# Optimization experiments

Hardware: AMD Instinct MI355X
Metric: run time of the kernel (lower is better)

## Reference

```python
import jax, jax.numpy as jnp
import numpy as np

PROJ_DIM = 8192
INPUT_DIM = 512
THRESH = 1e-08


def _signed_sqrt(x):
    return jnp.sign(x) * jnp.sqrt(jnp.abs(x))


def _make_sketch_matrix(key, input_dim, proj_dim):
    kh, ks = jax.random.split(key)
    h = jax.random.randint(kh, (input_dim,), 0, proj_dim)
    s = jnp.sign(jax.random.uniform(ks, (input_dim,), minval=-1.0, maxval=1.0)).astype(jnp.float32)
    M = jnp.zeros((input_dim, proj_dim), dtype=jnp.float32)
    return M.at[jnp.arange(input_dim), h].set(s)


def setup_inputs() -> dict:
    key = jax.random.key(0)
    kx, k1, k2 = jax.random.split(key, 3)
    x = jax.random.normal(kx, (32, 14, 14, INPUT_DIM), dtype=jnp.float32)
    M1 = _make_sketch_matrix(k1, INPUT_DIM, PROJ_DIM)
    M2 = _make_sketch_matrix(k2, INPUT_DIM, PROJ_DIM)
    return {"x": x, "M1": M1, "M2": M2}


def reference(x, M1, M2):
    B, H, W, C = x.shape
    x_flat = x.reshape(-1, C)                      # [B*H*W, C]
    # count-sketch projections (dense matmul, as in the original layer)
    p1 = (x_flat @ M1).astype(jnp.complex64)       # [B*H*W, P]
    p2 = (x_flat @ M2).astype(jnp.complex64)
    # circular convolution via FFT
    sketch = jnp.fft.fft(p1, axis=-1) * jnp.fft.fft(p2, axis=-1)
    y = jnp.real(jnp.fft.ifft(sketch, axis=-1)).astype(jnp.float32)
    y = y.reshape(B, H, W, -1).sum(axis=(1, 2))    # sum-pool over spatial dims -> [B, P]
    y = _signed_sqrt(y)
    # tf.nn.l2_normalize(x, axis=1, epsilon=1e-10)
    inv_norm = jax.lax.rsqrt(jnp.maximum(jnp.sum(y * y, axis=1, keepdims=True), 1e-10))
    return y * inv_norm
```

## Files before the change

kernel.cpp:

```cpp
#include <hip/hip_runtime.h>
#include <math.h>

#define PROJ 8192
#define CDIM 512
#define HWPOS 196
#define NBATCH 32
#define KPAD 224
#define NSLAB 7
#define NTP 10

typedef __attribute__((ext_vector_type(8))) short   short8;
typedef __attribute__((ext_vector_type(4))) float   f32x4;

__device__ __forceinline__ unsigned short f2bf(float f) {
    unsigned u = __float_as_uint(f);
    u += 0x7fff + ((u >> 16) & 1);
    return (unsigned short)(u >> 16);
}
__device__ __forceinline__ float bf2f(unsigned short h) {
    return __uint_as_float(((unsigned)h) << 16);
}

__global__ __launch_bounds__(256) void extract_kernel(
    const float* __restrict__ M1, const float* __restrict__ M2,
    int* __restrict__ h1, float* __restrict__ s1,
    int* __restrict__ h2, float* __restrict__ s2,
    float* __restrict__ norm)
{
    const int row = blockIdx.x;
    const float* M = blockIdx.y ? M2 : M1;
    int*   h = blockIdx.y ? h2 : h1;
    float* s = blockIdx.y ? s2 : s1;
    const float* mrow = M + (size_t)row * PROJ;

    if (blockIdx.x == 0 && blockIdx.y == 0 && threadIdx.x < NBATCH)
        norm[threadIdx.x] = 0.0f;

    for (int i = threadIdx.x * 4; i < PROJ; i += 256 * 4) {
        float4 v = *(const float4*)(mrow + i);
        if (v.x != 0.0f) { h[row] = i + 0; s[row] = v.x; }
        if (v.y != 0.0f) { h[row] = i + 1; s[row] = v.y; }
        if (v.z != 0.0f) { h[row] = i + 2; s[row] = v.z; }
        if (v.w != 0.0f) { h[row] = i + 3; s[row] = v.w; }
    }
}

__global__ __launch_bounds__(256) void prep_kernel(
    const float* __restrict__ x,
    unsigned short* __restrict__ XThi, unsigned short* __restrict__ XTlo)
{
    const int ks  = blockIdx.x;
    const int bat = blockIdx.y;
    const int tid = threadIdx.x;
    __shared__ float xt[32][513];

    const float* xb = x + (size_t)bat * HWPOS * CDIM;
    const int k0 = ks * 32;
#pragma unroll
    for (int i = 0; i < 16; ++i) {
        const int idx = i * 1024 + tid * 4;
        const int kr  = idx >> 9;
        const int c   = idx & 511;
        float4 v = make_float4(0.f, 0.f, 0.f, 0.f);
        if (k0 + kr < HWPOS) v = *(const float4*)(xb + (size_t)(k0 + kr) * CDIM + c);
        xt[kr][c+0] = v.x; xt[kr][c+1] = v.y; xt[kr][c+2] = v.z; xt[kr][c+3] = v.w;
    }
    __syncthreads();

    unsigned short* ohi = XThi + ((size_t)bat * NSLAB + ks) * 16384;
    unsigned short* olo = XTlo + ((size_t)bat * NSLAB + ks) * 16384;
#pragma unroll
    for (int i = 0; i < 8; ++i) {
        const int ch   = i * 256 + tid;
        const int c16  = ch & 15;
        const int quad = (ch >> 4) & 3;
        const int cgrp = ch >> 6;
        const int c    = cgrp * 16 + c16;
        short8 vh, vl;
#pragma unroll
        for (int j = 0; j < 8; ++j) {
            float f = xt[quad * 8 + j][c];
            unsigned short h = f2bf(f);
            vh[j] = (short)h;
            vl[j] = (short)f2bf(f - bf2f(h));
        }
        *(short8*)(ohi + ch * 8) = vh;
        *(short8*)(olo + ch * 8) = vl;
    }
}

__global__ __launch_bounds__(256) void gramscatter_kernel(
    const unsigned short* __restrict__ XThi, const unsigned short* __restrict__ XTlo,
    const int* __restrict__ h1, const float* __restrict__ s1,
    const int* __restrict__ h2, const float* __restrict__ s2,
    float* __restrict__ pbins)
{
    const int tp  = blockIdx.x;
    const int bat = blockIdx.y;
    const int bi  = (tp < 4) ? 0 : (tp < 7) ? 1 : (tp < 9) ? 2 : 3;
    const int bj  = (tp < 4) ? tp : (tp < 7) ? (tp - 3) : (tp < 9) ? (tp - 5) : 3;
    const int tid  = threadIdx.x;
    const int w    = tid >> 6;
    const int lane = tid & 63;

    __shared__ __align__(16) unsigned short Sbuf[4][4096];
    __shared__ float bins[PROJ];
    __shared__ int   th1[256]; __shared__ float ts1[256];
    __shared__ int   th2[256]; __shared__ float ts2[256];

    for (int i = tid; i < PROJ; i += 256) bins[i] = 0.f;
    {
        const int g = (tid < 128) ? (bi * 128 + tid) : (bj * 128 + tid - 128);
        th1[tid] = h1[g]; ts1[tid] = s1[g];
        th2[tid] = h2[g]; ts2[tid] = s2[g];
    }

    const int tile = (w < 2) ? bi : bj;
    const unsigned short* srcbase = ((w & 1) ? XTlo : XThi)
                                  + (size_t)bat * NSLAB * 16384 + (size_t)tile * 4096;
    const int rowq = w >> 1, colq = w & 1;

    f32x4 acc[16];
#pragma unroll
    for (int i = 0; i < 16; ++i) { acc[i][0]=0.f; acc[i][1]=0.f; acc[i][2]=0.f; acc[i][3]=0.f; }

    __syncthreads();

    for (int ks = 0; ks < NSLAB; ++ks) {
        const unsigned short* src = srcbase + (size_t)ks * 16384;
#pragma unroll
        for (int i = 0; i < 8; ++i) {
            const int off = i * 512 + lane * 8;
            *(short8*)&Sbuf[w][off] = *(const short8*)(src + off);
        }
        __syncthreads();

        short8 ah[4], al[4], bh[4], bl[4];
#pragma unroll
        for (int t = 0; t < 4; ++t) {
            ah[t] = *(const short8*)&Sbuf[0][(rowq * 4 + t) * 512 + lane * 8];
            al[t] = *(const short8*)&Sbuf[1][(rowq * 4 + t) * 512 + lane * 8];
            bh[t] = *(const short8*)&Sbuf[2][(colq * 4 + t) * 512 + lane * 8];
            bl[t] = *(const short8*)&Sbuf[3][(colq * 4 + t) * 512 + lane * 8];
        }
#pragma unroll
        for (int mt = 0; mt < 4; ++mt)
#pragma unroll
            for (int nt = 0; nt < 4; ++nt) {
                const int idx = mt * 4 + nt;
                acc[idx] = __builtin_amdgcn_mfma_f32_16x16x32_bf16(ah[mt], bh[nt], acc[idx], 0, 0, 0);
                acc[idx] = __builtin_amdgcn_mfma_f32_16x16x32_bf16(ah[mt], bl[nt], acc[idx], 0, 0, 0);
                acc[idx] = __builtin_amdgcn_mfma_f32_16x16x32_bf16(al[mt], bh[nt], acc[idx], 0, 0, 0);
            }
        __syncthreads();
    }

    const bool mirror = (bi != bj);
    int   h2c[4], h1c[4];
    float s2c[4], s1c[4];
#pragma unroll
    for (int nt = 0; nt < 4; ++nt) {
        const int cl = colq * 64 + nt * 16 + (lane & 15);
        h2c[nt] = th2[128 + cl]; s2c[nt] = ts2[128 + cl];
        h1c[nt] = th1[128 + cl]; s1c[nt] = ts1[128 + cl];
    }
    const int quad = lane >> 4;
#pragma unroll
    for (int mt = 0; mt < 4; ++mt)
#pragma unroll
        for (int reg = 0; reg < 4; ++reg) {
            const int rl = rowq * 64 + mt * 16 + quad * 4 + reg;
            const int   h1r = th1[rl]; const float s1r = ts1[rl];
            const int   h2r = th2[rl]; const float s2r = ts2[rl];
#pragma unroll
            for (int nt = 0; nt < 4; ++nt) {
                const float v = acc[mt * 4 + nt][reg];
                atomicAdd(&bins[(h1r + h2c[nt]) & (PROJ - 1)], s1r * s2c[nt] * v);
                if (mirror)
                    atomicAdd(&bins[(h1c[nt] + h2r) & (PROJ - 1)], s1c[nt] * s2r * v);
            }
        }
    __syncthreads();

    float* dst = pbins + ((size_t)bat * NTP + tp) * PROJ;
    for (int i = tid * 4; i < PROJ; i += 1024)
        *(float4*)(dst + i) = *(const float4*)&bins[i];
}

__global__ __launch_bounds__(256) void reduce_kernel(
    const float* __restrict__ pbins, float* __restrict__ out,
    float* __restrict__ norm)
{
    const int chunk = blockIdx.x;
    const int bat   = blockIdx.y;
    const int tid   = threadIdx.x;
    const int base  = chunk * 1024 + tid * 4;

    const float* pb = pbins + (size_t)bat * NTP * PROJ;
    float4 v = make_float4(0.f, 0.f, 0.f, 0.f);
#pragma unroll
    for (int t = 0; t < NTP; ++t) {
        float4 p = *(const float4*)(pb + (size_t)t * PROJ + base);
        v.x += p.x; v.y += p.y; v.z += p.z; v.w += p.w;
    }

    float4 sv;
    sv.x = (v.x >= 0.f) ? sqrtf(v.x) : -sqrtf(-v.x);
    sv.y = (v.y >= 0.f) ? sqrtf(v.y) : -sqrtf(-v.y);
    sv.z = (v.z >= 0.f) ? sqrtf(v.z) : -sqrtf(-v.z);
    sv.w = (v.w >= 0.f) ? sqrtf(v.w) : -sqrtf(-v.w);
    *(float4*)(out + (size_t)bat * PROJ + base) = sv;

    float local = fabsf(v.x) + fabsf(v.y) + fabsf(v.z) + fabsf(v.w);
#pragma unroll
    for (int off = 32; off > 0; off >>= 1) local += __shfl_down(local, off, 64);

    __shared__ float wred[4];
    if ((tid & 63) == 0) wred[tid >> 6] = local;
    __syncthreads();
    if (tid == 0)
        atomicAdd(&norm[bat], wred[0] + wred[1] + wred[2] + wred[3]);
}

__global__ __launch_bounds__(256) void normalize_kernel(
    float* __restrict__ out, const float* __restrict__ norm)
{
    const int bat = blockIdx.y;
    const int idx = blockIdx.x * 1024 + threadIdx.x * 4;
    const float inv = rsqrtf(fmaxf(norm[bat], 1e-10f));
    float4* p = (float4*)(out + (size_t)bat * PROJ + idx);
    float4 v = *p;
    v.x *= inv; v.y *= inv; v.z *= inv; v.w *= inv;
    *p = v;
}

extern "C" void kernel_launch(void* const* d_in, const int* in_sizes, int n_in,
                              void* d_out, int out_size, void* d_ws, size_t ws_size,
                              hipStream_t stream)
{
    const float* x  = (const float*)d_in[0];
    const float* M1 = (const float*)d_in[1];
    const float* M2 = (const float*)d_in[2];
    float* out = (float*)d_out;

    char* ws = (char*)d_ws;
    int*            h1    = (int*)   (ws + 0);
    float*          s1    = (float*) (ws + 2048);
    int*            h2    = (int*)   (ws + 4096);
    float*          s2    = (float*) (ws + 6144);
    float*          norm  = (float*) (ws + 8192);
    unsigned short* XThi  = (unsigned short*)(ws + 16384);
    unsigned short* XTlo  = (unsigned short*)(ws + 7356416);
    float*          pbins = (float*) (ws + 14696448);

    extract_kernel<<<dim3(512, 2), 256, 0, stream>>>(M1, M2, h1, s1, h2, s2, norm);
    prep_kernel<<<dim3(NSLAB, NBATCH), 256, 0, stream>>>(x, XThi, XTlo);
    gramscatter_kernel<<<dim3(NTP, NBATCH), 256, 0, stream>>>(XThi, XTlo, h1, s1, h2, s2, pbins);
    reduce_kernel<<<dim3(8, NBATCH), 256, 0, stream>>>(pbins, out, norm);
    normalize_kernel<<<dim3(8, NBATCH), 256, 0, stream>>>(out, norm);
}
```

Baseline: 195.0 us.

## Double-buffer gram tiles with async global-to-LDS loads and remap block grid

The gram-scatter kernel now double-buffers its LDS tiles and uses global_load_lds to prefetch the next K-slab while MFMAs run on the current one. This drops one barrier per iteration and hides global load latency. The launch becomes a flat grid with a remapped block-to-(tile,batch) order, which changes how blocks spread across XCDs and their L2 locality. Shared-memory atomics switch to unsafeAtomicAdd so hardware float atomics are used. The costs are doubled LDS staging, which may reduce occupancy, and reliance on the implicit waitcnt at the barrier for correctness.

```diff
diff --git a/kernel.cpp b/kernel.cpp
--- a/kernel.cpp
+++ b/kernel.cpp
@@ -5,7 +5,6 @@
 #define CDIM 512
 #define HWPOS 196
 #define NBATCH 32
-#define KPAD 224
 #define NSLAB 7
 #define NTP 10
 
@@ -95,18 +94,35 @@
     const int* __restrict__ h2, const float* __restrict__ s2,
     float* __restrict__ pbins)
 {
-    const int tp  = blockIdx.x;
-    const int bat = blockIdx.y;
+    const int id  = blockIdx.x;
+    const int sub = id >> 3;
+    const int tp  = sub % NTP;
+    const int bat = (id & 7) + 8 * (sub / NTP);
     const int bi  = (tp < 4) ? 0 : (tp < 7) ? 1 : (tp < 9) ? 2 : 3;
     const int bj  = (tp < 4) ? tp : (tp < 7) ? (tp - 3) : (tp < 9) ? (tp - 5) : 3;
     const int tid  = threadIdx.x;
     const int w    = tid >> 6;
     const int lane = tid & 63;
 
-    __shared__ __align__(16) unsigned short Sbuf[4][4096];
+    __shared__ __align__(16) unsigned short Sbuf[2][4][4096];
     __shared__ float bins[PROJ];
     __shared__ int   th1[256]; __shared__ float ts1[256];
     __shared__ int   th2[256]; __shared__ float ts2[256];
+
+    const int tile = (w < 2) ? bi : bj;
+    const unsigned short* srcbase = ((w & 1) ? XTlo : XThi)
+                                  + (size_t)bat * NSLAB * 16384 + (size_t)tile * 4096;
+    const int rowq = w >> 1, colq = w & 1;
+
+    {
+        const unsigned short* src = srcbase;
+        unsigned short* dst = &Sbuf[0][w][0];
+#pragma unroll
+        for (int i = 0; i < 8; ++i)
+            __builtin_amdgcn_global_load_lds(
+                (const __attribute__((address_space(1))) void*)(src + i * 512 + lane * 8),
+                (__attribute__((address_space(3))) void*)(dst + i * 512), 16, 0, 0);
+    }
 
     for (int i = tid; i < PROJ; i += 256) bins[i] = 0.f;
     {
@@ -115,33 +131,31 @@
         th2[tid] = h2[g]; ts2[tid] = s2[g];
     }
 
-    const int tile = (w < 2) ? bi : bj;
-    const unsigned short* srcbase = ((w & 1) ? XTlo : XThi)
-                                  + (size_t)bat * NSLAB * 16384 + (size_t)tile * 4096;
-    const int rowq = w >> 1, colq = w & 1;
-
     f32x4 acc[16];
 #pragma unroll
     for (int i = 0; i < 16; ++i) { acc[i][0]=0.f; acc[i][1]=0.f; acc[i][2]=0.f; acc[i][3]=0.f; }
 
-    __syncthreads();
-
     for (int ks = 0; ks < NSLAB; ++ks) {
-        const unsigned short* src = srcbase + (size_t)ks * 16384;
-#pragma unroll
-        for (int i = 0; i < 8; ++i) {
-            const int off = i * 512 + lane * 8;
-            *(short8*)&Sbuf[w][off] = *(const short8*)(src + off);
-        }
         __syncthreads();
+        const int buf = ks & 1;
+
+        if (ks + 1 < NSLAB) {
+            const unsigned short* src = srcbase + (size_t)(ks + 1) * 16384;
+            unsigned short* dst = &Sbuf[buf ^ 1][w][0];
+#pragma unroll
+            for (int i = 0; i < 8; ++i)
+                __builtin_amdgcn_global_load_lds(
+                    (const __attribute__((address_space(1))) void*)(src + i * 512 + lane * 8),
+                    (__attribute__((address_space(3))) void*)(dst + i * 512), 16, 0, 0);
+        }
 
         short8 ah[4], al[4], bh[4], bl[4];
 #pragma unroll
         for (int t = 0; t < 4; ++t) {
-            ah[t] = *(const short8*)&Sbuf[0][(rowq * 4 + t) * 512 + lane * 8];
-            al[t] = *(const short8*)&Sbuf[1][(rowq * 4 + t) * 512 + lane * 8];
-            bh[t] = *(const short8*)&Sbuf[2][(colq * 4 + t) * 512 + lane * 8];
-            bl[t] = *(const short8*)&Sbuf[3][(colq * 4 + t) * 512 + lane * 8];
+            ah[t] = *(const short8*)&Sbuf[buf][0][(rowq * 4 + t) * 512 + lane * 8];
+            al[t] = *(const short8*)&Sbuf[buf][1][(rowq * 4 + t) * 512 + lane * 8];
+            bh[t] = *(const short8*)&Sbuf[buf][2][(colq * 4 + t) * 512 + lane * 8];
+            bl[t] = *(const short8*)&Sbuf[buf][3][(colq * 4 + t) * 512 + lane * 8];
         }
 #pragma unroll
         for (int mt = 0; mt < 4; ++mt)
@@ -152,7 +166,6 @@
                 acc[idx] = __builtin_amdgcn_mfma_f32_16x16x32_bf16(ah[mt], bl[nt], acc[idx], 0, 0, 0);
                 acc[idx] = __builtin_amdgcn_mfma_f32_16x16x32_bf16(al[mt], bh[nt], acc[idx], 0, 0, 0);
             }
-        __syncthreads();
     }
 
     const bool mirror = (bi != bj);
@@ -175,9 +188,9 @@
 #pragma unroll
             for (int nt = 0; nt < 4; ++nt) {
                 const float v = acc[mt * 4 + nt][reg];
-                atomicAdd(&bins[(h1r + h2c[nt]) & (PROJ - 1)], s1r * s2c[nt] * v);
+                unsafeAtomicAdd(&bins[(h1r + h2c[nt]) & (PROJ - 1)], s1r * s2c[nt] * v);
                 if (mirror)
-                    atomicAdd(&bins[(h1c[nt] + h2r) & (PROJ - 1)], s1c[nt] * s2r * v);
+                    unsafeAtomicAdd(&bins[(h1c[nt] + h2r) & (PROJ - 1)], s1c[nt] * s2r * v);
             }
         }
     __syncthreads();
@@ -219,7 +232,7 @@
     if ((tid & 63) == 0) wred[tid >> 6] = local;
     __syncthreads();
     if (tid == 0)
-        atomicAdd(&norm[bat], wred[0] + wred[1] + wred[2] + wred[3]);
+        unsafeAtomicAdd(&norm[bat], wred[0] + wred[1] + wred[2] + wred[3]);
 }
 
 __global__ __launch_bounds__(256) void normalize_kernel(
@@ -255,7 +268,7 @@
 
     extract_kernel<<<dim3(512, 2), 256, 0, stream>>>(M1, M2, h1, s1, h2, s2, norm);
     prep_kernel<<<dim3(NSLAB, NBATCH), 256, 0, stream>>>(x, XThi, XTlo);
-    gramscatter_kernel<<<dim3(NTP, NBATCH), 256, 0, stream>>>(XThi, XTlo, h1, s1, h2, s2, pbins);
+    gramscatter_kernel<<<NTP * NBATCH, 256, 0, stream>>>(XThi, XTlo, h1, s1, h2, s2, pbins);
     reduce_kernel<<<dim3(8, NBATCH), 256, 0, stream>>>(pbins, out, norm);
     normalize_kernel<<<dim3(8, NBATCH), 256, 0, stream>>>(out, norm);
 }
```

Measured after the change: 185.2 us. -5.0%, faster.
